# Kernel optimization log

Measured on AMD Instinct MI355X. Metric: run time of the kernel, lower is better.

Reference implementation:

```python
import jax, jax.numpy as jnp
import numpy as np

DIM = 256
NUM_HEADS = 8
NUM_PATCH = (80, 64)
WIN = (5, 2)
NUM_MLP = 256  # must equal DIM for residual add
EPS = 1e-5


def _rel_pos_index():
    wh, ww = WIN
    coords_h = np.arange(wh)
    coords_w = np.arange(ww)
    coords = np.stack(np.meshgrid(coords_h, coords_w, indexing='ij'))  # [2,wh,ww]
    flat = coords.reshape(2, -1)  # [2, wh*ww]
    rel = flat[:, :, None] - flat[:, None, :]  # [2, N, N]
    rel = rel.transpose(1, 2, 0)
    rel[:, :, 0] += wh - 1
    rel[:, :, 1] += ww - 1
    rel[:, :, 0] *= 2 * ww - 1
    return rel.sum(-1).astype(np.int32)  # [N, N]

REL_IDX = jnp.asarray(_rel_pos_index())


def layernorm(x, g, b):
    m = jnp.mean(x, axis=-1, keepdims=True)
    v = jnp.var(x, axis=-1, keepdims=True)
    return (x - m) * jax.lax.rsqrt(v + EPS) * g + b


def setup_inputs() -> dict:
    key = jax.random.key(0)
    ks = jax.random.split(key, 12)
    B = 32
    L = NUM_PATCH[0] * NUM_PATCH[1]
    s = lambda k, shp: jax.random.normal(k, shp, dtype=jnp.float32) * 0.02
    n_bias = (2 * WIN[0] - 1) * (2 * WIN[1] - 1)
    return {
        'x': jax.random.normal(ks[0], (B, L, DIM), dtype=jnp.float32),
        'norm1_g': jnp.ones((DIM,), jnp.float32),
        'norm1_b': jnp.zeros((DIM,), jnp.float32),
        'rel_bias_table': s(ks[1], (n_bias, NUM_HEADS)),
        'proj_w': s(ks[2], (DIM, DIM)),
        'proj_b': jnp.zeros((DIM,), jnp.float32),
        'norm2_g': jnp.ones((DIM,), jnp.float32),
        'norm2_b': jnp.zeros((DIM,), jnp.float32),
        'mlp1_w': s(ks[3], (DIM, DIM)),
        'mlp1_b': jnp.zeros((DIM,), jnp.float32),
        'mlp2_w': s(ks[4], (DIM, NUM_MLP)),
        'mlp2_b': jnp.zeros((NUM_MLP,), jnp.float32),
    }


def _forward(x, norm1_g, norm1_b, rel_bias_table, proj_w, proj_b,
             norm2_g, norm2_b, mlp1_w, mlp1_b, mlp2_w, mlp2_b):
    B, L, C = x.shape
    H, W = NUM_PATCH
    wh, ww = WIN
    N = wh * ww
    hd = C // NUM_HEADS
    scale = hd ** (-0.5)

    x_skip = x
    h = layernorm(x, norm1_g, norm1_b)
    h = h.reshape(B, H // wh, wh, W // ww, ww, C)
    # -> windows [B*nW, N, C]
    h = h.transpose(0, 1, 3, 2, 4, 5).reshape(-1, N, C)

    # NOTE: faithful to source quirk — q=k=v = reshaped input (qkv Dense unused)
    qkv = h.reshape(-1, N, NUM_HEADS, hd).transpose(0, 2, 1, 3)  # [BW, nh, N, hd]
    attn = jnp.einsum('bhqd,bhkd->bhqk', qkv * scale, qkv)
    bias = rel_bias_table[REL_IDX.reshape(-1)].reshape(N, N, NUM_HEADS)
    attn = attn + bias.transpose(2, 0, 1)[None]
    attn = jax.nn.softmax(attn, axis=-1)
    out = jnp.einsum('bhqk,bhkd->bhqd', attn, qkv)
    out = out.transpose(0, 2, 1, 3).reshape(-1, N, C)
    # NOTE: source WindowAttention never applies self.proj; faithful omission

    out = out.reshape(B, H // wh, W // ww, wh, ww, C)
    out = out.transpose(0, 1, 3, 2, 4, 5).reshape(B, L, C)
    x = x_skip + out

    x_skip = x
    h = layernorm(x, norm2_g, norm2_b)
    h = jax.nn.gelu(h @ mlp1_w + mlp1_b, approximate=False)
    h = h @ mlp2_w + mlp2_b
    return x_skip + h


def reference(x, norm1_g, norm1_b, rel_bias_table, proj_w, proj_b,
              norm2_g, norm2_b, mlp1_w, mlp1_b, mlp2_w, mlp2_b):
    return _forward(x, norm1_g, norm1_b, rel_bias_table, proj_w, proj_b,
                    norm2_g, norm2_b, mlp1_w, mlp1_b, mlp2_w, mlp2_b)
```

## Files before the change

### kernel.cpp

```cpp
#include <hip/hip_runtime.h>
#include <hip/hip_bf16.h>
#include <math.h>

#define DIM 256
#define NHEAD 8
#define HD 32
#define WH 5
#define WW 2
#define NTOK 10
#define WPAT 64
#define LTOK 5120
#define EPS 1e-5f

typedef __attribute__((ext_vector_type(8))) short bh8;
typedef __attribute__((ext_vector_type(4))) short sh4;
typedef __attribute__((ext_vector_type(4))) float fx4;

__device__ inline unsigned short f2bf(float f) {
    unsigned int u = __builtin_bit_cast(unsigned int, f);
    u += 0x7fffu + ((u >> 16) & 1u);
    return (unsigned short)(u >> 16);
}

__device__ inline float wave_reduce_sum(float v) {
    #pragma unroll
    for (int off = 32; off > 0; off >>= 1) v += __shfl_xor(v, off);
    return v;
}

__global__ void prep_kernel(const float* __restrict__ w1,
                            const float* __restrict__ w2,
                            unsigned short* __restrict__ wtf) {
    int gid = blockIdx.x * 256 + threadIdx.x;
    int lane = gid & 63;
    int ko = (gid >> 6) & 7;
    int ni = (gid >> 9) & 3;
    int s  = (gid >> 11) & 3;
    int mat = gid >> 13;
    const float* src = mat ? w2 : w1;
    int col = s * 64 + ni * 16 + (lane & 15);
    int k0 = ko * 32 + (lane >> 4) * 8;
    unsigned short* dst = wtf + (size_t)gid * 8;
    #pragma unroll
    for (int j = 0; j < 8; ++j)
        dst[j] = f2bf(src[(k0 + j) * 256 + col]);
}

__global__ __launch_bounds__(256) void attn_kernel(
    const float* __restrict__ x, const float* __restrict__ g1,
    const float* __restrict__ b1, const float* __restrict__ btab,
    float* __restrict__ x1) {
    __shared__ float xs[NTOK][DIM + 8];
    __shared__ float hs[NTOK][DIM + 8];
    __shared__ float pm[NHEAD * NTOK * NTOK];

    int w = blockIdx.x;
    int b = w >> 9;
    int rh = (w >> 5) & 15;
    int cw = w & 31;
    int tid = threadIdx.x;
    int lane = tid & 63;
    int wave = tid >> 6;
    long base = (long)b * LTOK + rh * (WH * WPAT) + cw * WW;

    #pragma unroll
    for (int i = 0; i < WH; ++i) {
        const float2* src = (const float2*)(x + (base + (long)i * WPAT) * DIM);
        float2 v = src[tid];
        int p = tid * 2;
        int tok = i * 2 + (p >> 8);
        int c = p & 255;
        *(float2*)&xs[tok][c] = v;
    }
    __syncthreads();

    float4 g4 = *(const float4*)(g1 + lane * 4);
    float4 b4 = *(const float4*)(b1 + lane * 4);
    for (int tok = wave; tok < NTOK; tok += 4) {
        float4 v = *(const float4*)&xs[tok][lane * 4];
        float s = v.x + v.y + v.z + v.w;
        float q = v.x * v.x + v.y * v.y + v.z * v.z + v.w * v.w;
        s = wave_reduce_sum(s);
        q = wave_reduce_sum(q);
        float mean = s * (1.0f / DIM);
        float var = q * (1.0f / DIM) - mean * mean;
        float rstd = rsqrtf(var + EPS);
        float4 h;
        h.x = (v.x - mean) * rstd * g4.x + b4.x;
        h.y = (v.y - mean) * rstd * g4.y + b4.y;
        h.z = (v.z - mean) * rstd * g4.z + b4.z;
        h.w = (v.w - mean) * rstd * g4.w + b4.w;
        *(float4*)&hs[tok][lane * 4] = h;
    }
    __syncthreads();

    const float scale = 0.17677669529663689f;
    for (int item = tid; item < NHEAD * NTOK * NTOK; item += 256) {
        int head = item / 100;
        int rem = item - head * 100;
        int q = rem / 10;
        int k = rem - q * 10;
        float acc = 0.f;
        #pragma unroll
        for (int d = 0; d < HD; ++d)
            acc += hs[q][head * HD + d] * hs[k][head * HD + d];
        int iq = q >> 1, jq = q & 1, ik = k >> 1, jk = k & 1;
        int bidx = (iq - ik + WH - 1) * (2 * WW - 1) + (jq - jk + WW - 1);
        pm[item] = acc * scale + btab[bidx * NHEAD + head];
    }
    __syncthreads();

    if (tid < NHEAD * NTOK) {
        float* row = pm + tid * NTOK;
        float m = row[0];
        #pragma unroll
        for (int k = 1; k < NTOK; ++k) m = fmaxf(m, row[k]);
        float e[NTOK];
        float s = 0.f;
        #pragma unroll
        for (int k = 0; k < NTOK; ++k) { e[k] = __expf(row[k] - m); s += e[k]; }
        float inv = 1.0f / s;
        #pragma unroll
        for (int k = 0; k < NTOK; ++k) row[k] = e[k] * inv;
    }
    __syncthreads();

    int head = tid >> 5;
    float hv[NTOK];
    #pragma unroll
    for (int k = 0; k < NTOK; ++k) hv[k] = hs[k][tid];
    #pragma unroll
    for (int q = 0; q < NTOK; ++q) {
        const float* pr = pm + (head * NTOK + q) * NTOK;
        float acc = 0.f;
        #pragma unroll
        for (int k = 0; k < NTOK; ++k) acc += pr[k] * hv[k];
        float o = xs[q][tid] + acc;
        long l = base + (q >> 1) * WPAT + (q & 1);
        x1[l * DIM + tid] = o;
    }
}

__global__ __launch_bounds__(256, 2) void mlp_kernel(
    float* __restrict__ xio,
    const float* __restrict__ g2, const float* __restrict__ b2,
    const unsigned short* __restrict__ wtf,
    const float* __restrict__ mb1, const float* __restrict__ mb2) {
    __shared__ unsigned short As[64][DIM + 8];

    int m0 = blockIdx.x * 64;
    int tid = threadIdx.x;
    int lane = tid & 63;
    int wave = tid >> 6;
    int lr = lane & 15;
    int lk = lane >> 4;
    int n0 = wave * 64;

    const unsigned short* w1base = wtf + (size_t)wave * 16384 + (size_t)lane * 8;
    const unsigned short* w2base = wtf + 65536 + (size_t)wave * 16384 + (size_t)lane * 8;

    int r = tid >> 2;
    int q = tid & 3;
    const float4* rowp = (const float4*)(xio + (long)(m0 + r) * DIM);
    float4 v[16];
    #pragma unroll
    for (int i = 0; i < 16; ++i) v[i] = rowp[q + 4 * i];

    bh8 wf[4][8];
    #pragma unroll
    for (int ni = 0; ni < 4; ++ni)
        #pragma unroll
        for (int ko = 0; ko < 8; ++ko)
            wf[ni][ko] = *(const bh8*)(w1base + (size_t)(ni * 8 + ko) * 512);

    float bias1v[4];
    #pragma unroll
    for (int ni = 0; ni < 4; ++ni) bias1v[ni] = mb1[n0 + ni * 16 + lr];

    {
        float s = 0.f, sq = 0.f;
        #pragma unroll
        for (int i = 0; i < 16; ++i) {
            s += v[i].x + v[i].y + v[i].z + v[i].w;
            sq += v[i].x * v[i].x + v[i].y * v[i].y + v[i].z * v[i].z + v[i].w * v[i].w;
        }
        s += __shfl_xor(s, 1);  s += __shfl_xor(s, 2);
        sq += __shfl_xor(sq, 1); sq += __shfl_xor(sq, 2);
        float mean = s * (1.0f / DIM);
        float var = sq * (1.0f / DIM) - mean * mean;
        float rstd = rsqrtf(var + EPS);

        const float4* g4p = (const float4*)g2;
        const float4* b4p = (const float4*)b2;
        #pragma unroll
        for (int i = 0; i < 16; ++i) {
            int c4 = q + 4 * i;
            float4 gg = g4p[c4];
            float4 bb = b4p[c4];
            sh4 h;
            h.x = (short)f2bf((v[i].x - mean) * rstd * gg.x + bb.x);
            h.y = (short)f2bf((v[i].y - mean) * rstd * gg.y + bb.y);
            h.z = (short)f2bf((v[i].z - mean) * rstd * gg.z + bb.z);
            h.w = (short)f2bf((v[i].w - mean) * rstd * gg.w + bb.w);
            *(sh4*)&As[r][c4 * 4] = h;
        }
    }
    __syncthreads();

    const fx4 zero = {0.f, 0.f, 0.f, 0.f};

    fx4 acc[4][4];
    #pragma unroll
    for (int mi = 0; mi < 4; ++mi)
        #pragma unroll
        for (int ni = 0; ni < 4; ++ni) acc[mi][ni] = zero;

    #pragma unroll
    for (int ko = 0; ko < 8; ++ko) {
        bh8 a[4];
        #pragma unroll
        for (int mi = 0; mi < 4; ++mi)
            a[mi] = *(const bh8*)&As[mi * 16 + lr][ko * 32 + lk * 8];
        #pragma unroll
        for (int mi = 0; mi < 4; ++mi)
            #pragma unroll
            for (int ni = 0; ni < 4; ++ni)
                acc[mi][ni] = __builtin_amdgcn_mfma_f32_16x16x32_bf16(a[mi], wf[ni][ko], acc[mi][ni], 0, 0, 0);
    }
    __syncthreads();

    #pragma unroll
    for (int ni = 0; ni < 4; ++ni)
        #pragma unroll
        for (int ko = 0; ko < 8; ++ko)
            wf[ni][ko] = *(const bh8*)(w2base + (size_t)(ni * 8 + ko) * 512);

    float bias2v[4];
    #pragma unroll
    for (int ni = 0; ni < 4; ++ni) bias2v[ni] = mb2[n0 + ni * 16 + lr];

    #pragma unroll
    for (int mi = 0; mi < 4; ++mi)
        #pragma unroll
        for (int ni = 0; ni < 4; ++ni)
            #pragma unroll
            for (int rr = 0; rr < 4; ++rr) {
                float vv = acc[mi][ni][rr] + bias1v[ni];
                float t = 0.7978845608028654f * (vv + 0.044715f * vv * vv * vv);
                float ge = vv / (1.0f + __expf(-2.0f * t));
                As[mi * 16 + lk * 4 + rr][n0 + ni * 16 + lr] = f2bf(ge);
            }
    __syncthreads();

    fx4 acc2[4][4];
    #pragma unroll
    for (int mi = 0; mi < 4; ++mi)
        #pragma unroll
        for (int ni = 0; ni < 4; ++ni) acc2[mi][ni] = zero;

    #pragma unroll
    for (int ko = 0; ko < 8; ++ko) {
        bh8 a[4];
        #pragma unroll
        for (int mi = 0; mi < 4; ++mi)
            a[mi] = *(const bh8*)&As[mi * 16 + lr][ko * 32 + lk * 8];
        #pragma unroll
        for (int mi = 0; mi < 4; ++mi)
            #pragma unroll
            for (int ni = 0; ni < 4; ++ni)
                acc2[mi][ni] = __builtin_amdgcn_mfma_f32_16x16x32_bf16(a[mi], wf[ni][ko], acc2[mi][ni], 0, 0, 0);
    }

    #pragma unroll
    for (int mi = 0; mi < 4; ++mi)
        #pragma unroll
        for (int ni = 0; ni < 4; ++ni)
            #pragma unroll
            for (int rr = 0; rr < 4; ++rr) {
                long row = m0 + mi * 16 + lk * 4 + rr;
                int col = n0 + ni * 16 + lr;
                long idx = row * DIM + col;
                xio[idx] = xio[idx] + acc2[mi][ni][rr] + bias2v[ni];
            }
}

extern "C" void kernel_launch(void* const* d_in, const int* in_sizes, int n_in,
                              void* d_out, int out_size, void* d_ws, size_t ws_size,
                              hipStream_t stream) {
    const float* x    = (const float*)d_in[0];
    const float* g1   = (const float*)d_in[1];
    const float* b1   = (const float*)d_in[2];
    const float* btab = (const float*)d_in[3];
    const float* g2   = (const float*)d_in[6];
    const float* b2   = (const float*)d_in[7];
    const float* w1   = (const float*)d_in[8];
    const float* mb1  = (const float*)d_in[9];
    const float* w2   = (const float*)d_in[10];
    const float* mb2  = (const float*)d_in[11];
    float* out = (float*)d_out;
    unsigned short* wtf = (unsigned short*)d_ws;

    prep_kernel<<<64, 256, 0, stream>>>(w1, w2, wtf);
    attn_kernel<<<16384, 256, 0, stream>>>(x, g1, b1, btab, out);
    mlp_kernel<<<2560, 256, 0, stream>>>(out, g2, b2, wtf, mb1, mb2);
}
```

Baseline: 202.5 us.

## Fuse window attention and MLP into one kernel with bf16 LDS residual

Replaces the separate attention and MLP kernels with a single kernel where each 512-thread block handles 16 windows (160 tokens), keeping the attention output in LDS as bf16 and feeding it straight into the two MFMA GEMMs. This removes the round trip of the intermediate activation through global memory and one kernel launch. Attention is restructured so each wave computes per-head dot products with shuffle reductions over registers. The residual x1 is now stored in bf16, which lowers accuracy. Weights are streamed from global per k-step instead of held in registers, and there are only 1024 blocks, which may limit occupancy.

```diff
diff --git a/kernel.cpp b/kernel.cpp
--- a/kernel.cpp
+++ b/kernel.cpp
@@ -4,28 +4,22 @@
 
 #define DIM 256
 #define NHEAD 8
-#define HD 32
-#define WH 5
-#define WW 2
 #define NTOK 10
-#define WPAT 64
 #define LTOK 5120
 #define EPS 1e-5f
 
 typedef __attribute__((ext_vector_type(8))) short bh8;
 typedef __attribute__((ext_vector_type(4))) short sh4;
 typedef __attribute__((ext_vector_type(4))) float fx4;
+typedef unsigned short LRow[DIM + 8];
 
 __device__ inline unsigned short f2bf(float f) {
     unsigned int u = __builtin_bit_cast(unsigned int, f);
     u += 0x7fffu + ((u >> 16) & 1u);
     return (unsigned short)(u >> 16);
 }
-
-__device__ inline float wave_reduce_sum(float v) {
-    #pragma unroll
-    for (int off = 32; off > 0; off >>= 1) v += __shfl_xor(v, off);
-    return v;
+__device__ inline float bf2f(unsigned short h) {
+    return __builtin_bit_cast(float, (unsigned int)h << 16);
 }
 
 __global__ void prep_kernel(const float* __restrict__ w1,
@@ -46,242 +40,255 @@
         dst[j] = f2bf(src[(k0 + j) * 256 + col]);
 }
 
-__global__ __launch_bounds__(256) void attn_kernel(
+__global__ __launch_bounds__(512) void fused_kernel(
     const float* __restrict__ x, const float* __restrict__ g1,
     const float* __restrict__ b1, const float* __restrict__ btab,
-    float* __restrict__ x1) {
-    __shared__ float xs[NTOK][DIM + 8];
-    __shared__ float hs[NTOK][DIM + 8];
-    __shared__ float pm[NHEAD * NTOK * NTOK];
-
-    int w = blockIdx.x;
-    int b = w >> 9;
-    int rh = (w >> 5) & 15;
-    int cw = w & 31;
+    const float* __restrict__ g2, const float* __restrict__ b2,
+    const unsigned short* __restrict__ wtf,
+    const float* __restrict__ mb1, const float* __restrict__ mb2,
+    float* __restrict__ out) {
+
+    __shared__ unsigned short x1t[160][DIM + 8];
+    __shared__ __align__(16) char scratch[33792];
+    __shared__ float biasT[216];
+
+    float (*pmw)[800] = (float (*)[800])scratch;
+    LRow* As2 = (LRow*)scratch;
+    LRow* h1t = (LRow*)(scratch + sizeof(LRow) * 32);
+
     int tid = threadIdx.x;
     int lane = tid & 63;
-    int wave = tid >> 6;
-    long base = (long)b * LTOK + rh * (WH * WPAT) + cw * WW;
-
+    int w = tid >> 6;
+
+    int blk = blockIdx.x;
+    int b = blk >> 5;
+    int rh = (blk >> 1) & 15;
+    int hf = blk & 1;
+    size_t tb = (size_t)b * LTOK + (size_t)(rh * 5) * 64 + hf * 32;
+
+    if (tid < 216) biasT[tid] = btab[tid];
     #pragma unroll
-    for (int i = 0; i < WH; ++i) {
-        const float2* src = (const float2*)(x + (base + (long)i * WPAT) * DIM);
-        float2 v = src[tid];
-        int p = tid * 2;
-        int tok = i * 2 + (p >> 8);
-        int c = p & 255;
-        *(float2*)&xs[tok][c] = v;
+    for (int it = 0; it < 20; ++it) {
+        int t = tid + it * 512;
+        int r = t >> 6;
+        int qd = t & 63;
+        const float4 v = *(const float4*)(x + (tb + (size_t)(r >> 5) * 64 + (r & 31)) * DIM + qd * 4);
+        sh4 hh;
+        hh.x = (short)f2bf(v.x); hh.y = (short)f2bf(v.y);
+        hh.z = (short)f2bf(v.z); hh.w = (short)f2bf(v.w);
+        *(sh4*)&x1t[r][qd * 4] = hh;
     }
     __syncthreads();
 
-    float4 g4 = *(const float4*)(g1 + lane * 4);
-    float4 b4 = *(const float4*)(b1 + lane * 4);
-    for (int tok = wave; tok < NTOK; tok += 4) {
-        float4 v = *(const float4*)&xs[tok][lane * 4];
-        float s = v.x + v.y + v.z + v.w;
-        float q = v.x * v.x + v.y * v.y + v.z * v.z + v.w * v.w;
-        s = wave_reduce_sum(s);
-        q = wave_reduce_sum(q);
-        float mean = s * (1.0f / DIM);
-        float var = q * (1.0f / DIM) - mean * mean;
-        float rstd = rsqrtf(var + EPS);
-        float4 h;
-        h.x = (v.x - mean) * rstd * g4.x + b4.x;
-        h.y = (v.y - mean) * rstd * g4.y + b4.y;
-        h.z = (v.z - mean) * rstd * g4.z + b4.z;
-        h.w = (v.w - mean) * rstd * g4.w + b4.w;
-        *(float4*)&hs[tok][lane * 4] = h;
+    {
+        int hd = lane >> 3;
+        float g4x[4], b4x[4];
+        {
+            const float4 gg = *(const float4*)(g1 + lane * 4);
+            const float4 bb = *(const float4*)(b1 + lane * 4);
+            g4x[0] = gg.x; g4x[1] = gg.y; g4x[2] = gg.z; g4x[3] = gg.w;
+            b4x[0] = bb.x; b4x[1] = bb.y; b4x[2] = bb.z; b4x[3] = bb.w;
+        }
+        float* pw = pmw[w];
+        const float scale = 0.17677669529663689f;
+
+        for (int wd2 = 0; wd2 < 2; ++wd2) {
+            int colb = (w * 2 + wd2) * 2;
+
+            float hs[NTOK][4];
+            #pragma unroll
+            for (int tk = 0; tk < NTOK; ++tk) {
+                int rt = (tk >> 1) * 32 + colb + (tk & 1);
+                sh4 xv = *(const sh4*)&x1t[rt][lane * 4];
+                float f0 = bf2f((unsigned short)xv.x);
+                float f1 = bf2f((unsigned short)xv.y);
+                float f2 = bf2f((unsigned short)xv.z);
+                float f3 = bf2f((unsigned short)xv.w);
+                float s = f0 + f1 + f2 + f3;
+                float sq = f0 * f0 + f1 * f1 + f2 * f2 + f3 * f3;
+                #pragma unroll
+                for (int off = 32; off > 0; off >>= 1) {
+                    s += __shfl_xor(s, off);
+                    sq += __shfl_xor(sq, off);
+                }
+                float mean = s * (1.0f / DIM);
+                float rstd = rsqrtf(sq * (1.0f / DIM) - mean * mean + EPS);
+                hs[tk][0] = (f0 - mean) * rstd * g4x[0] + b4x[0];
+                hs[tk][1] = (f1 - mean) * rstd * g4x[1] + b4x[1];
+                hs[tk][2] = (f2 - mean) * rstd * g4x[2] + b4x[2];
+                hs[tk][3] = (f3 - mean) * rstd * g4x[3] + b4x[3];
+            }
+
+            #pragma unroll
+            for (int q = 0; q < NTOK; ++q)
+                #pragma unroll
+                for (int k = 0; k < NTOK; ++k) {
+                    float p = hs[q][0] * hs[k][0] + hs[q][1] * hs[k][1]
+                            + hs[q][2] * hs[k][2] + hs[q][3] * hs[k][3];
+                    p += __shfl_xor(p, 1);
+                    p += __shfl_xor(p, 2);
+                    p += __shfl_xor(p, 4);
+                    int bidx = ((q >> 1) - (k >> 1) + 4) * 3 + ((q & 1) - (k & 1) + 1);
+                    if ((lane & 7) == 0)
+                        pw[(hd * NTOK + q) * NTOK + k] = p * scale + biasT[bidx * 8 + hd];
+                }
+            __syncthreads();
+
+            {
+                float* row = pw + lane * NTOK;
+                float m = row[0];
+                #pragma unroll
+                for (int k = 1; k < NTOK; ++k) m = fmaxf(m, row[k]);
+                float e[NTOK]; float s = 0.f;
+                #pragma unroll
+                for (int k = 0; k < NTOK; ++k) { e[k] = __expf(row[k] - m); s += e[k]; }
+                float inv = 1.0f / s;
+                #pragma unroll
+                for (int k = 0; k < NTOK; ++k) row[k] = e[k] * inv;
+            }
+            if (lane < 16) {
+                float* row = pw + (64 + lane) * NTOK;
+                float m = row[0];
+                #pragma unroll
+                for (int k = 1; k < NTOK; ++k) m = fmaxf(m, row[k]);
+                float e[NTOK]; float s = 0.f;
+                #pragma unroll
+                for (int k = 0; k < NTOK; ++k) { e[k] = __expf(row[k] - m); s += e[k]; }
+                float inv = 1.0f / s;
+                #pragma unroll
+                for (int k = 0; k < NTOK; ++k) row[k] = e[k] * inv;
+            }
+            __syncthreads();
+
+            #pragma unroll
+            for (int q = 0; q < NTOK; ++q) {
+                float a0 = 0.f, a1 = 0.f, a2 = 0.f, a3 = 0.f;
+                #pragma unroll
+                for (int k = 0; k < NTOK; ++k) {
+                    float pv = pw[(hd * NTOK + q) * NTOK + k];
+                    a0 += pv * hs[k][0]; a1 += pv * hs[k][1];
+                    a2 += pv * hs[k][2]; a3 += pv * hs[k][3];
+                }
+                int rt = (q >> 1) * 32 + colb + (q & 1);
+                sh4 xv = *(const sh4*)&x1t[rt][lane * 4];
+                sh4 o;
+                o.x = (short)f2bf(bf2f((unsigned short)xv.x) + a0);
+                o.y = (short)f2bf(bf2f((unsigned short)xv.y) + a1);
+                o.z = (short)f2bf(bf2f((unsigned short)xv.z) + a2);
+                o.w = (short)f2bf(bf2f((unsigned short)xv.w) + a3);
+                *(sh4*)&x1t[rt][lane * 4] = o;
+            }
+            __syncthreads();
+        }
     }
     __syncthreads();
 
-    const float scale = 0.17677669529663689f;
-    for (int item = tid; item < NHEAD * NTOK * NTOK; item += 256) {
-        int head = item / 100;
-        int rem = item - head * 100;
-        int q = rem / 10;
-        int k = rem - q * 10;
-        float acc = 0.f;
-        #pragma unroll
-        for (int d = 0; d < HD; ++d)
-            acc += hs[q][head * HD + d] * hs[k][head * HD + d];
-        int iq = q >> 1, jq = q & 1, ik = k >> 1, jk = k & 1;
-        int bidx = (iq - ik + WH - 1) * (2 * WW - 1) + (jq - jk + WW - 1);
-        pm[item] = acc * scale + btab[bidx * NHEAD + head];
-    }
-    __syncthreads();
-
-    if (tid < NHEAD * NTOK) {
-        float* row = pm + tid * NTOK;
-        float m = row[0];
-        #pragma unroll
-        for (int k = 1; k < NTOK; ++k) m = fmaxf(m, row[k]);
-        float e[NTOK];
-        float s = 0.f;
-        #pragma unroll
-        for (int k = 0; k < NTOK; ++k) { e[k] = __expf(row[k] - m); s += e[k]; }
-        float inv = 1.0f / s;
-        #pragma unroll
-        for (int k = 0; k < NTOK; ++k) row[k] = e[k] * inv;
-    }
-    __syncthreads();
-
-    int head = tid >> 5;
-    float hv[NTOK];
+    int rr = tid >> 4;
+    int qq = tid & 15;
+    float g2v[16], b2v[16];
+    {
+        const float4* gp = (const float4*)(g2 + qq * 16);
+        const float4* bp = (const float4*)(b2 + qq * 16);
+        #pragma unroll
+        for (int u = 0; u < 4; ++u) {
+            float4 gg = gp[u], bb = bp[u];
+            g2v[u * 4] = gg.x; g2v[u * 4 + 1] = gg.y; g2v[u * 4 + 2] = gg.z; g2v[u * 4 + 3] = gg.w;
+            b2v[u * 4] = bb.x; b2v[u * 4 + 1] = bb.y; b2v[u * 4 + 2] = bb.z; b2v[u * 4 + 3] = bb.w;
+        }
+    }
+    int lr = lane & 15, lk = lane >> 4;
+    int mt = w >> 2;
+    int ns = w & 3;
+    const unsigned short* w1base = wtf + (size_t)ns * 16384 + (size_t)lane * 8;
+    const unsigned short* w2base = w1base + 65536;
+    float bias1v[4], bias2v[4];
     #pragma unroll
-    for (int k = 0; k < NTOK; ++k) hv[k] = hs[k][tid];
-    #pragma unroll
-    for (int q = 0; q < NTOK; ++q) {
-        const float* pr = pm + (head * NTOK + q) * NTOK;
-        float acc = 0.f;
-        #pragma unroll
-        for (int k = 0; k < NTOK; ++k) acc += pr[k] * hv[k];
-        float o = xs[q][tid] + acc;
-        long l = base + (q >> 1) * WPAT + (q & 1);
-        x1[l * DIM + tid] = o;
-    }
-}
-
-__global__ __launch_bounds__(256, 2) void mlp_kernel(
-    float* __restrict__ xio,
-    const float* __restrict__ g2, const float* __restrict__ b2,
-    const unsigned short* __restrict__ wtf,
-    const float* __restrict__ mb1, const float* __restrict__ mb2) {
-    __shared__ unsigned short As[64][DIM + 8];
-
-    int m0 = blockIdx.x * 64;
-    int tid = threadIdx.x;
-    int lane = tid & 63;
-    int wave = tid >> 6;
-    int lr = lane & 15;
-    int lk = lane >> 4;
-    int n0 = wave * 64;
-
-    const unsigned short* w1base = wtf + (size_t)wave * 16384 + (size_t)lane * 8;
-    const unsigned short* w2base = wtf + 65536 + (size_t)wave * 16384 + (size_t)lane * 8;
-
-    int r = tid >> 2;
-    int q = tid & 3;
-    const float4* rowp = (const float4*)(xio + (long)(m0 + r) * DIM);
-    float4 v[16];
-    #pragma unroll
-    for (int i = 0; i < 16; ++i) v[i] = rowp[q + 4 * i];
-
-    bh8 wf[4][8];
-    #pragma unroll
-    for (int ni = 0; ni < 4; ++ni)
-        #pragma unroll
-        for (int ko = 0; ko < 8; ++ko)
-            wf[ni][ko] = *(const bh8*)(w1base + (size_t)(ni * 8 + ko) * 512);
-
-    float bias1v[4];
-    #pragma unroll
-    for (int ni = 0; ni < 4; ++ni) bias1v[ni] = mb1[n0 + ni * 16 + lr];
-
-    {
-        float s = 0.f, sq = 0.f;
-        #pragma unroll
-        for (int i = 0; i < 16; ++i) {
-            s += v[i].x + v[i].y + v[i].z + v[i].w;
-            sq += v[i].x * v[i].x + v[i].y * v[i].y + v[i].z * v[i].z + v[i].w * v[i].w;
-        }
-        s += __shfl_xor(s, 1);  s += __shfl_xor(s, 2);
-        sq += __shfl_xor(sq, 1); sq += __shfl_xor(sq, 2);
-        float mean = s * (1.0f / DIM);
-        float var = sq * (1.0f / DIM) - mean * mean;
-        float rstd = rsqrtf(var + EPS);
-
-        const float4* g4p = (const float4*)g2;
-        const float4* b4p = (const float4*)b2;
-        #pragma unroll
-        for (int i = 0; i < 16; ++i) {
-            int c4 = q + 4 * i;
-            float4 gg = g4p[c4];
-            float4 bb = b4p[c4];
-            sh4 h;
-            h.x = (short)f2bf((v[i].x - mean) * rstd * gg.x + bb.x);
-            h.y = (short)f2bf((v[i].y - mean) * rstd * gg.y + bb.y);
-            h.z = (short)f2bf((v[i].z - mean) * rstd * gg.z + bb.z);
-            h.w = (short)f2bf((v[i].w - mean) * rstd * gg.w + bb.w);
-            *(sh4*)&As[r][c4 * 4] = h;
-        }
-    }
-    __syncthreads();
-
+    for (int ni = 0; ni < 4; ++ni) {
+        bias1v[ni] = mb1[ns * 64 + ni * 16 + lr];
+        bias2v[ni] = mb2[ns * 64 + ni * 16 + lr];
+    }
     const fx4 zero = {0.f, 0.f, 0.f, 0.f};
 
-    fx4 acc[4][4];
-    #pragma unroll
-    for (int mi = 0; mi < 4; ++mi)
-        #pragma unroll
-        for (int ni = 0; ni < 4; ++ni) acc[mi][ni] = zero;
-
-    #pragma unroll
-    for (int ko = 0; ko < 8; ++ko) {
-        bh8 a[4];
-        #pragma unroll
-        for (int mi = 0; mi < 4; ++mi)
-            a[mi] = *(const bh8*)&As[mi * 16 + lr][ko * 32 + lk * 8];
-        #pragma unroll
-        for (int mi = 0; mi < 4; ++mi)
+    for (int c = 0; c < 5; ++c) {
+        {
+            bh8 v0 = *(const bh8*)&x1t[c * 32 + rr][qq * 16];
+            bh8 v1 = *(const bh8*)&x1t[c * 32 + rr][qq * 16 + 8];
+            float f[16];
+            #pragma unroll
+            for (int e = 0; e < 8; ++e) {
+                f[e] = bf2f((unsigned short)v0[e]);
+                f[8 + e] = bf2f((unsigned short)v1[e]);
+            }
+            float sm = 0.f, sq = 0.f;
+            #pragma unroll
+            for (int e = 0; e < 16; ++e) { sm += f[e]; sq += f[e] * f[e]; }
+            sm += __shfl_xor(sm, 1); sm += __shfl_xor(sm, 2); sm += __shfl_xor(sm, 4); sm += __shfl_xor(sm, 8);
+            sq += __shfl_xor(sq, 1); sq += __shfl_xor(sq, 2); sq += __shfl_xor(sq, 4); sq += __shfl_xor(sq, 8);
+            float mean = sm * (1.0f / DIM);
+            float rstd = rsqrtf(sq * (1.0f / DIM) - mean * mean + EPS);
+            bh8 h0, h1v;
+            #pragma unroll
+            for (int e = 0; e < 8; ++e) {
+                h0[e] = (short)f2bf((f[e] - mean) * rstd * g2v[e] + b2v[e]);
+                h1v[e] = (short)f2bf((f[8 + e] - mean) * rstd * g2v[8 + e] + b2v[8 + e]);
+            }
+            *(bh8*)&As2[rr][qq * 16] = h0;
+            *(bh8*)&As2[rr][qq * 16 + 8] = h1v;
+        }
+        __syncthreads();
+
+        fx4 acc[4];
+        #pragma unroll
+        for (int ni = 0; ni < 4; ++ni) acc[ni] = zero;
+        #pragma unroll
+        for (int ko = 0; ko < 8; ++ko) {
+            bh8 wfv[4];
             #pragma unroll
             for (int ni = 0; ni < 4; ++ni)
-                acc[mi][ni] = __builtin_amdgcn_mfma_f32_16x16x32_bf16(a[mi], wf[ni][ko], acc[mi][ni], 0, 0, 0);
-    }
-    __syncthreads();
-
-    #pragma unroll
-    for (int ni = 0; ni < 4; ++ni)
-        #pragma unroll
-        for (int ko = 0; ko < 8; ++ko)
-            wf[ni][ko] = *(const bh8*)(w2base + (size_t)(ni * 8 + ko) * 512);
-
-    float bias2v[4];
-    #pragma unroll
-    for (int ni = 0; ni < 4; ++ni) bias2v[ni] = mb2[n0 + ni * 16 + lr];
-
-    #pragma unroll
-    for (int mi = 0; mi < 4; ++mi)
+                wfv[ni] = *(const bh8*)(w1base + (size_t)(ni * 8 + ko) * 512);
+            bh8 a = *(const bh8*)&As2[mt * 16 + lr][ko * 32 + lk * 8];
+            #pragma unroll
+            for (int ni = 0; ni < 4; ++ni)
+                acc[ni] = __builtin_amdgcn_mfma_f32_16x16x32_bf16(a, wfv[ni], acc[ni], 0, 0, 0);
+        }
+
         #pragma unroll
         for (int ni = 0; ni < 4; ++ni)
             #pragma unroll
-            for (int rr = 0; rr < 4; ++rr) {
-                float vv = acc[mi][ni][rr] + bias1v[ni];
-                float t = 0.7978845608028654f * (vv + 0.044715f * vv * vv * vv);
-                float ge = vv / (1.0f + __expf(-2.0f * t));
-                As[mi * 16 + lk * 4 + rr][n0 + ni * 16 + lr] = f2bf(ge);
-            }
-    __syncthreads();
-
-    fx4 acc2[4][4];
-    #pragma unroll
-    for (int mi = 0; mi < 4; ++mi)
-        #pragma unroll
-        for (int ni = 0; ni < 4; ++ni) acc2[mi][ni] = zero;
-
-    #pragma unroll
-    for (int ko = 0; ko < 8; ++ko) {
-        bh8 a[4];
-        #pragma unroll
-        for (int mi = 0; mi < 4; ++mi)
-            a[mi] = *(const bh8*)&As[mi * 16 + lr][ko * 32 + lk * 8];
-        #pragma unroll
-        for (int mi = 0; mi < 4; ++mi)
+            for (int r4 = 0; r4 < 4; ++r4) {
+                float vv = acc[ni][r4] + bias1v[ni];
+                float t2 = 0.7978845608028654f * (vv + 0.044715f * vv * vv * vv);
+                float ge = vv / (1.0f + __expf(-2.0f * t2));
+                h1t[mt * 16 + lk * 4 + r4][ns * 64 + ni * 16 + lr] = f2bf(ge);
+            }
+        __syncthreads();
+
+        fx4 acc2[4];
+        #pragma unroll
+        for (int ni = 0; ni < 4; ++ni) acc2[ni] = zero;
+        #pragma unroll
+        for (int ko = 0; ko < 8; ++ko) {
+            bh8 wfv[4];
             #pragma unroll
             for (int ni = 0; ni < 4; ++ni)
-                acc2[mi][ni] = __builtin_amdgcn_mfma_f32_16x16x32_bf16(a[mi], wf[ni][ko], acc2[mi][ni], 0, 0, 0);
-    }
-
-    #pragma unroll
-    for (int mi = 0; mi < 4; ++mi)
+                wfv[ni] = *(const bh8*)(w2base + (size_t)(ni * 8 + ko) * 512);
+            bh8 a = *(const bh8*)&h1t[mt * 16 + lr][ko * 32 + lk * 8];
+            #pragma unroll
+            for (int ni = 0; ni < 4; ++ni)
+                acc2[ni] = __builtin_amdgcn_mfma_f32_16x16x32_bf16(a, wfv[ni], acc2[ni], 0, 0, 0);
+        }
+
         #pragma unroll
         for (int ni = 0; ni < 4; ++ni)
             #pragma unroll
-            for (int rr = 0; rr < 4; ++rr) {
-                long row = m0 + mi * 16 + lk * 4 + rr;
-                int col = n0 + ni * 16 + lr;
-                long idx = row * DIM + col;
-                xio[idx] = xio[idx] + acc2[mi][ni][rr] + bias2v[ni];
-            }
+            for (int r4 = 0; r4 < 4; ++r4) {
+                int row32 = mt * 16 + lk * 4 + r4;
+                int col = ns * 64 + ni * 16 + lr;
+                float resid = bf2f(x1t[c * 32 + row32][col]);
+                out[(tb + (size_t)c * 64 + row32) * DIM + col] = resid + acc2[ni][r4] + bias2v[ni];
+            }
+        __syncthreads();
+    }
 }
 
 extern "C" void kernel_launch(void* const* d_in, const int* in_sizes, int n_in,
@@ -301,6 +308,5 @@
     unsigned short* wtf = (unsigned short*)d_ws;
 
     prep_kernel<<<64, 256, 0, stream>>>(w1, w2, wtf);
-    attn_kernel<<<16384, 256, 0, stream>>>(x, g1, b1, btab, out);
-    mlp_kernel<<<2560, 256, 0, stream>>>(out, g2, b2, wtf, mb1, mb2);
-}
+    fused_kernel<<<1024, 512, 0, stream>>>(x, g1, b1, btab, g2, b2, wtf, mb1, mb2, out);
+}
```

After: 426.4 us. 111% more time.
